# Kernel tuning notes

Hardware: AMD Instinct MI355X
Metric: run time of the kernel (lower is better)

The kernel has to match this reference:

```python
import jax, jax.numpy as jnp
import numpy as np

B, N, C, F, OUT = 4, 512, 1024, 1024, 1024
LOC = 128  # min(128, out_channels)
EPS_BN = 1e-5


def _batchnorm(x, g, b):
    # BatchNorm1d in training mode: biased batch stats over rows
    m = jnp.mean(x, axis=0)
    v = jnp.var(x, axis=0)
    return (x - m) / jnp.sqrt(v + EPS_BN) * g + b


def _relative_pe(loc):
    # loc: [N,4] (x,y,w,h) -> [N,N,LOC]; faithfully replicates the torch
    # cat([N,4N]) -> view(-1,4) interleaving of the original code.
    cx = loc[:, 0] + 0.5 * loc[:, 2]
    cy = loc[:, 1] + 0.5 * loc[:, 3]
    w, h = loc[:, 2], loc[:, 3]
    eps = jnp.float32(1e-3)
    dx = jnp.maximum(jnp.abs(cx[:, None] - cx[None, :]) / w[None, :], eps)
    dy = jnp.maximum(jnp.abs(cy[:, None] - cy[None, :]) / h[None, :], eps)
    dw = w[:, None] / w[None, :]
    dh = h[:, None] / h[None, :]
    delta = jnp.log(jnp.concatenate([dx, dy, dw, dh], axis=-1))  # [N,4N]
    delta = delta.reshape(-1, 4)                                  # [N*N,4]
    d = LOC // 8
    pe = jnp.exp(2.0 * jnp.arange(d, dtype=jnp.float32) / d * np.log(1000.0))
    ang = delta[:, :, None] / pe                                  # [N*N,4,d]
    emb = jnp.concatenate([jnp.sin(ang), jnp.cos(ang)], axis=-1)  # [N*N,4,2d]
    return emb.reshape(N, N, LOC)


def reference(box_features, boxes, bn1_g, bn1_b, Wq, bq, Wk, bk, Wv, bv, Wr, br, bn2_g, bn2_b):
    feat = _batchnorm(box_features, bn1_g, bn1_b).reshape(B, N, C)

    def per_image(f, loc):
        rel = jnp.squeeze(_relative_pe(loc) @ Wr + br, axis=-1)   # [N,N]
        q = f @ Wq + bq
        k = f @ Wk + bk
        v = f @ Wv + bv
        att = q @ k.T / jnp.sqrt(jnp.float32(F)) + jax.nn.log_softmax(rel, axis=-1)
        return jax.nn.softmax(att, axis=-1) @ v                   # [N,OUT]

    out = jax.vmap(per_image)(feat, boxes).reshape(B * N, OUT)
    return _batchnorm(out, bn2_g, bn2_b)


def setup_inputs() -> dict:
    key = jax.random.key(0)
    ks = jax.random.split(key, 10)
    box_features = jax.random.normal(ks[0], (B * N, C), dtype=jnp.float32)
    u = jax.random.uniform(ks[1], (B, N, 4), dtype=jnp.float32)
    xy = u[..., :2] * 800.0
    wh = 16.0 + u[..., 2:] * 240.0
    boxes = jnp.concatenate([xy, wh], axis=-1)
    s = 0.02
    return {
        "box_features": box_features,
        "boxes": boxes,
        "bn1_g": jnp.ones((C,), jnp.float32),
        "bn1_b": jnp.zeros((C,), jnp.float32),
        "Wq": jax.random.normal(ks[2], (C, F), jnp.float32) * s,
        "bq": jnp.zeros((F,), jnp.float32),
        "Wk": jax.random.normal(ks[3], (C, F), jnp.float32) * s,
        "bk": jnp.zeros((F,), jnp.float32),
        "Wv": jax.random.normal(ks[4], (C, OUT), jnp.float32) * s,
        "bv": jnp.zeros((OUT,), jnp.float32),
        "Wr": jax.random.normal(ks[5], (LOC, 1), jnp.float32) * s,
        "br": jnp.zeros((1,), jnp.float32),
        "bn2_g": jnp.ones((OUT,), jnp.float32),
        "bn2_b": jnp.zeros((OUT,), jnp.float32),
    }
```

## Files before the change

kernel.cpp:

```cpp
#include <hip/hip_runtime.h>
#include <math.h>

typedef __bf16 bf16;
typedef __attribute__((ext_vector_type(8))) __bf16 bf16x8;
typedef __attribute__((ext_vector_type(4))) __bf16 bf16x4;
typedef __attribute__((ext_vector_type(4))) float f32x4;

#define NCH1 128
#define RPC1 16

#define XD0   (-6.93f)
#define XSPAN (11.03f)
#define XINVH (1023.f / 11.03f)

__global__ __launch_bounds__(256)
void prep(const float* __restrict__ Wq, const float* __restrict__ Wk, const float* __restrict__ Wv,
          bf16* __restrict__ T0, bf16* __restrict__ T1, bf16* __restrict__ T2,
          const float* __restrict__ bq, const float* __restrict__ bk, float* __restrict__ biasqk,
          const float* __restrict__ X, float* __restrict__ psum, float* __restrict__ psq,
          const float* __restrict__ boxes, const float* __restrict__ Wr, const float* __restrict__ br,
          float* __restrict__ ent, float* __restrict__ tabs)
{
    __shared__ float tile[64][65];
    const int bid = blockIdx.x;
    const int tid = threadIdx.x;

    if (bid < 768) {
        const int mat = bid >> 8, g2 = bid & 255;
        const float* W = (mat == 0) ? Wq : (mat == 1) ? Wk : Wv;
        bf16* T        = (mat == 0) ? T0 : (mat == 1) ? T1 : T2;
        const int bx = (g2 & 15) * 64, by = (g2 >> 4) * 64;
        const int tx = tid & 63, ty = tid >> 6;
#pragma unroll
        for (int i = 0; i < 16; ++i)
            tile[ty + i * 4][tx] = W[(long)(by + ty + i * 4) * 1024 + bx + tx];
        __syncthreads();
#pragma unroll
        for (int i = 0; i < 16; ++i)
            T[(long)(bx + ty + i * 4) * 1024 + by + tx] = (bf16)tile[tx][ty + i * 4];
    } else if (bid < 896) {
        const int c4 = tid;
        const long r0 = (long)(bid - 768) * RPC1;
        const float4* Xv = (const float4*)X;
        float4 s = {0.f,0.f,0.f,0.f}, q = {0.f,0.f,0.f,0.f};
#pragma unroll
        for (int r = 0; r < RPC1; ++r) {
            float4 x = Xv[(r0 + r) * 256 + c4];
            s.x += x.x; s.y += x.y; s.z += x.z; s.w += x.w;
            q.x += x.x*x.x; q.y += x.y*x.y; q.z += x.z*x.z; q.w += x.w*x.w;
        }
        ((float4*)psum)[(bid - 768) * 256 + c4] = s;
        ((float4*)psq) [(bid - 768) * 256 + c4] = q;
    } else if (bid == 896) {
        for (int e = tid; e < 2048; e += 256) {
            float4 b4 = ((const float4*)boxes)[e];
            float w = b4.z, h = b4.w;
            ent[0*2048+e] = b4.x + 0.5f * w;
            ent[1*2048+e] = b4.y + 0.5f * h;
            ent[2*2048+e] = __logf(w);
            ent[3*2048+e] = __logf(h);
            ent[4*2048+e] = 1e-3f * w;
            ent[5*2048+e] = 1e-3f * h;
        }
        for (int i = tid; i < 2048; i += 256)
            biasqk[i] = (i < 1024) ? bq[i] : bk[i - 1024];
    } else {
        const int c = bid - 897;
        float* tb = tabs + c * 1024;
        const float brq = 0.25f * br[0];
        const float hstep = XSPAN / 1023.f;
        for (int e = tid; e < 1024; e += 256) {
            float d = XD0 + hstep * (float)e;
            float a = brq;
#pragma unroll
            for (int k = 0; k < 16; ++k) {
                float tk = exp2f(-1.24572303558f * (float)k);
                float s_, c_;
                __sincosf(d * tk, &s_, &c_);
                a += s_ * Wr[c * 32 + k] + c_ * Wr[c * 32 + 16 + k];
            }
            tb[e] = a;
        }
    }
}

template <int NCH_, int BF16OUT>
__global__ __launch_bounds__(256)
void bn_final_apply(const float* __restrict__ X, const float* __restrict__ psum,
                    const float* __restrict__ psq, const float* __restrict__ g,
                    const float* __restrict__ b, void* __restrict__ Yp)
{
    __shared__ float ls[4][64], lq[4][64], ssc[64], ssh[64];
    const int t  = threadIdx.x;
    const int cs = blockIdx.x;
    const int rc = blockIdx.y;
    const int col_l = t & 63, part = t >> 6;
    const int col = cs * 64 + col_l;
    constexpr int CPT = NCH_ / 4;
    float s = 0.f, q = 0.f;
#pragma unroll
    for (int i = 0; i < CPT; ++i) {
        int ch = part * CPT + i;
        s += psum[ch * 1024 + col];
        q += psq [ch * 1024 + col];
    }
    ls[part][col_l] = s; lq[part][col_l] = q;
    __syncthreads();
    if (t < 64) {
        float S = ls[0][t]+ls[1][t]+ls[2][t]+ls[3][t];
        float Q = lq[0][t]+lq[1][t]+lq[2][t]+lq[3][t];
        float m = S / 2048.f;
        float v = Q / 2048.f - m*m;
        float inv = 1.0f / sqrtf(v + 1e-5f);
        float sc = g[cs*64+t] * inv;
        ssc[t] = sc; ssh[t] = b[cs*64+t] - m*sc;
    }
    __syncthreads();
    const int f = t & 15, rsub = t >> 4;
    float4 sc4 = ((const float4*)ssc)[f];
    float4 sh4 = ((const float4*)ssh)[f];
#pragma unroll
    for (int it = 0; it < 8; ++it) {
        int row = rc*128 + it*16 + rsub;
        float4 x = ((const float4*)(X + (long)row*1024 + cs*64))[f];
        float4 rv;
        rv.x = x.x*sc4.x + sh4.x;
        rv.y = x.y*sc4.y + sh4.y;
        rv.z = x.z*sc4.z + sh4.z;
        rv.w = x.w*sc4.w + sh4.w;
        if constexpr (BF16OUT) {
            bf16x4 y;
            y[0]=(bf16)rv.x; y[1]=(bf16)rv.y; y[2]=(bf16)rv.z; y[3]=(bf16)rv.w;
            ((bf16x4*)((bf16*)Yp + (long)row*1024 + cs*64))[f] = y;
        } else {
            ((float4*)((float*)Yp + (long)row*1024 + cs*64))[f] = rv;
        }
    }
}

__device__ __forceinline__ float look(const float* tab, float d)
{
    float t = (d - XD0) * XINVH;
    t = fminf(fmaxf(t, 0.f), 1022.999f);
    float fi = floorf(t);
    int i = (int)fi;
    float a = tab[i], b = tab[i + 1];
    return a + (b - a) * (t - fi);
}

__device__ __forceinline__ void stage_tile_128x32(const bf16* __restrict__ src_base, int ld,
                                                  int row0, int k0, bf16* lds_base, int w, int l)
{
#pragma unroll
    for (int t = 0; t < 2; ++t) {
        int rchunk = w * 32 + t * 16;
        const bf16* src = src_base + (long)(row0 + rchunk + (l >> 2)) * ld + k0 + (l & 3) * 8;
        __builtin_amdgcn_global_load_lds((__attribute__((address_space(1))) void*)src,
                                         (__attribute__((address_space(3))) void*)(lds_base + rchunk * 32),
                                         16, 0, 0);
    }
}

__device__ __forceinline__ void stage64(const bf16* __restrict__ src_base, int ld,
                                        int row0, int k0, bf16* lds_base, int w, int l)
{
    const bf16* src = src_base + (long)(row0 + w * 16 + (l >> 2)) * ld + k0 + (l & 3) * 8;
    __builtin_amdgcn_global_load_lds((__attribute__((address_space(1))) void*)src,
                                     (__attribute__((address_space(3))) void*)(lds_base + w * 16 * 32),
                                     16, 0, 0);
}

template <int MODE>
__device__ __forceinline__ void gemm_12864(
    const bf16* __restrict__ Ab, int lda, const bf16* __restrict__ Bb, int ldb,
    bf16* __restrict__ Cp, int ldc, int K, int bm, int bn,
    const float* __restrict__ bias, char* smem)
{
    bf16* As0 = (bf16*)smem;
    bf16* Bs0 = (bf16*)(smem + 16384);
    const int tid = threadIdx.x;
    const int w = tid >> 6, l = tid & 63;
    const int wr = w >> 1, wc = w & 1;

    f32x4 acc[4][2];
#pragma unroll
    for (int i = 0; i < 4; ++i)
#pragma unroll
        for (int j = 0; j < 2; ++j) acc[i][j] = (f32x4){0.f,0.f,0.f,0.f};

    const int nkt = K >> 5;
    stage_tile_128x32(Ab, lda, bm, 0, As0, w, l);
    stage64(Bb, ldb, bn, 0, Bs0, w, l);
    __syncthreads();

    const int fr = l & 15;
    const int ko = (l >> 4) * 8;

    for (int kt = 0; kt < nkt; ++kt) {
        const int cur = kt & 1;
        bf16* Asc = As0 + cur * 4096;
        bf16* Bsc = Bs0 + cur * 2048;
        if (kt + 1 < nkt) {
            stage_tile_128x32(Ab, lda, bm, (kt + 1) << 5, As0 + (cur ^ 1) * 4096, w, l);
            stage64(Bb, ldb, bn, (kt + 1) << 5, Bs0 + (cur ^ 1) * 2048, w, l);
        }
        bf16x8 af[4], bfv[2];
#pragma unroll
        for (int mi = 0; mi < 4; ++mi)
            af[mi] = *(const bf16x8*)(&Asc[(wr * 64 + mi * 16 + fr) * 32 + ko]);
#pragma unroll
        for (int ni = 0; ni < 2; ++ni)
            bfv[ni] = *(const bf16x8*)(&Bsc[(wc * 32 + ni * 16 + fr) * 32 + ko]);
#pragma unroll
        for (int mi = 0; mi < 4; ++mi)
#pragma unroll
            for (int ni = 0; ni < 2; ++ni)
                acc[mi][ni] = __builtin_amdgcn_mfma_f32_16x16x32_bf16(af[mi], bfv[ni], acc[mi][ni], 0, 0, 0);
        __syncthreads();
    }

    const int crow0 = bm + wr * 64 + (l >> 4) * 4;
    const int ccol0 = bn + wc * 32 + fr;
#pragma unroll
    for (int mi = 0; mi < 4; ++mi)
#pragma unroll
        for (int ni = 0; ni < 2; ++ni)
#pragma unroll
            for (int r = 0; r < 4; ++r) {
                const int row = crow0 + mi * 16 + r;
                const int col = ccol0 + ni * 16;
                const float v = acc[mi][ni][r];
                if constexpr (MODE == 0) {
                    Cp[(long)row * ldc + col] = (bf16)(v + bias[col]);
                } else {
                    Cp[(long)row * ldc + col] = (bf16)(v + bias[row]);
                }
            }
}

__global__ __launch_bounds__(256, 4)
void megaGEMM(const bf16* __restrict__ featbf, const bf16* __restrict__ WqkT,
              const bf16* __restrict__ WvT, bf16* __restrict__ qkbf, bf16* __restrict__ vTbf,
              const float* __restrict__ biasqk, const float* __restrict__ bv)
{
    __shared__ char smem[24576];
    const unsigned bid = blockIdx.x;
    const unsigned g = bid / 3u, r = bid % 3u;
    if (r < 2) {
        const unsigned t = g * 2 + r;
        gemm_12864<0>(featbf, 1024, WqkT, 1024, qkbf, 2048, 1024,
                      (t & 15) * 128, (t >> 4) * 64, biasqk, smem);
    } else {
        const int img = g >> 6, rem = g & 63;
        gemm_12864<1>(WvT, 1024, featbf + (long)img * 524288,  1024,
                      vTbf + (long)img * 524288, 512, 1024,
                      (rem >> 3) * 128, (rem & 7) * 64, bv, smem);
    }
}

__global__ __launch_bounds__(256, 4)
void attn64(const bf16* __restrict__ qk, float* __restrict__ S0, float* __restrict__ S1,
            const float* __restrict__ ent, const float* __restrict__ tabs)
{
    __shared__ char smem[20480];
    const int img = blockIdx.z >> 1, kh = blockIdx.z & 1;
    const int bm = blockIdx.x * 64, bn = blockIdx.y * 64;
    const bf16* A = qk + (long)img * 1048576 + kh * 512;
    const bf16* B = qk + 1024 + (long)img * 1048576 + kh * 512;
    bf16* As0 = (bf16*)smem;
    bf16* Bs0 = (bf16*)(smem + 8192);

    const int tid = threadIdx.x;
    const int w = tid >> 6, l = tid & 63;
    const int wr = w >> 1, wc = w & 1;
    const int fr = l & 15;
    const int ko = (l >> 4) * 8;

    f32x4 acc[2][2];
#pragma unroll
    for (int i = 0; i < 2; ++i)
#pragma unroll
        for (int j = 0; j < 2; ++j) acc[i][j] = (f32x4){0.f,0.f,0.f,0.f};

    stage64(A, 2048, bm, 0, As0, w, l);
    stage64(B, 2048, bn, 0, Bs0, w, l);
    __syncthreads();

    for (int kt = 0; kt < 16; ++kt) {
        const int cur = kt & 1;
        bf16* Asc = As0 + cur * 2048;
        bf16* Bsc = Bs0 + cur * 2048;
        if (kt + 1 < 16) {
            stage64(A, 2048, bm, (kt + 1) << 5, As0 + (cur ^ 1) * 2048, w, l);
            stage64(B, 2048, bn, (kt + 1) << 5, Bs0 + (cur ^ 1) * 2048, w, l);
        }
        bf16x8 af[2], bfv[2];
#pragma unroll
        for (int mi = 0; mi < 2; ++mi)
            af[mi] = *(const bf16x8*)(&Asc[(wr * 32 + mi * 16 + fr) * 32 + ko]);
#pragma unroll
        for (int ni = 0; ni < 2; ++ni)
            bfv[ni] = *(const bf16x8*)(&Bsc[(wc * 32 + ni * 16 + fr) * 32 + ko]);
#pragma unroll
        for (int mi = 0; mi < 2; ++mi)
#pragma unroll
            for (int ni = 0; ni < 2; ++ni)
                acc[mi][ni] = __builtin_amdgcn_mfma_f32_16x16x32_bf16(af[mi], bfv[ni], acc[mi][ni], 0, 0, 0);
        __syncthreads();
    }

    const float scale = 0.03125f;
    float* Sout = (kh == 0 ? S0 : S1) + (long)img * 262144;

    if (kh == 1) {
#pragma unroll
        for (int mi = 0; mi < 2; ++mi)
#pragma unroll
            for (int ni = 0; ni < 2; ++ni)
#pragma unroll
                for (int r = 0; r < 4; ++r) {
                    const int rowl = wr * 32 + mi * 16 + (l >> 4) * 4 + r;
                    const int coll = wc * 32 + ni * 16 + fr;
                    Sout[(long)(bm + rowl) * 512 + bn + coll] = acc[mi][ni][r] * scale;
                }
        return;
    }

    float* stab = (float*)smem;
    float* RA   = stab + 4096;
    float* SA   = RA + 64;
    float* SE   = SA + 260;
    float* SL   = SE + 260;
    const int b   = bn >> 7;
    const int jj0 = (bn & 64) * 4;
    for (int i = tid; i < 4096; i += 256) stab[i] = tabs[i];
    {
        const int eb = img * 512;
        if (tid < 64) RA[tid] = ent[b * 2048 + eb + bm + tid];
        for (int u = tid; u < 260 && jj0 + u < 512; u += 256) {
            SA[u] = ent[b * 2048 + eb + jj0 + u];
            if (b < 2) {
                SE[u] = ent[(4 + b) * 2048 + eb + jj0 + u];
                SL[u] = ent[(2 + b) * 2048 + eb + jj0 + u];
            }
        }
    }
    __syncthreads();
#pragma unroll
    for (int ni = 0; ni < 2; ++ni) {
        const int coll = wc * 32 + ni * 16 + fr;
        const int u0   = 4 * coll;
        const float sA0 = SA[u0], sA1 = SA[u0+1], sA2 = SA[u0+2], sA3 = SA[u0+3];
        float sE0=0.f,sE1=0.f,sE2=0.f,sE3=0.f, sL0=0.f,sL1=0.f,sL2=0.f,sL3=0.f;
        if (b < 2) {
            sE0 = SE[u0]; sE1 = SE[u0+1]; sE2 = SE[u0+2]; sE3 = SE[u0+3];
            sL0 = SL[u0]; sL1 = SL[u0+1]; sL2 = SL[u0+2]; sL3 = SL[u0+3];
        }
#pragma unroll
        for (int mi = 0; mi < 2; ++mi)
#pragma unroll
            for (int r = 0; r < 4; ++r) {
                const int rowl = wr * 32 + mi * 16 + (l >> 4) * 4 + r;
                const float ai = RA[rowl];
                float d0, d1, d2, d3;
                if (b < 2) {
                    d0 = __logf(fmaxf(fabsf(ai - sA0), sE0)) - sL0;
                    d1 = __logf(fmaxf(fabsf(ai - sA1), sE1)) - sL1;
                    d2 = __logf(fmaxf(fabsf(ai - sA2), sE2)) - sL2;
                    d3 = __logf(fmaxf(fabsf(ai - sA3), sE3)) - sL3;
                } else {
                    d0 = ai - sA0; d1 = ai - sA1; d2 = ai - sA2; d3 = ai - sA3;
                }
                float relv = look(stab,        d0) + look(stab + 1024, d1)
                           + look(stab + 2048, d2) + look(stab + 3072, d3);
                Sout[(long)(bm + rowl) * 512 + bn + coll] = acc[mi][ni][r] * scale + relv;
            }
    }
}

__global__ __launch_bounds__(256)
void softmax2(const float* __restrict__ S0, const float* __restrict__ S1, bf16* __restrict__ P)
{
    const long row = blockIdx.x;
    const int t = threadIdx.x;
    float x0 = S0[row * 512 + t]       + S1[row * 512 + t];
    float x1 = S0[row * 512 + t + 256] + S1[row * 512 + t + 256];
    float mx = fmaxf(x0, x1);
#pragma unroll
    for (int off = 32; off; off >>= 1) mx = fmaxf(mx, __shfl_xor(mx, off));
    __shared__ float redm[4], reds[4];
    if ((t & 63) == 0) redm[t >> 6] = mx;
    __syncthreads();
    mx = fmaxf(fmaxf(redm[0], redm[1]), fmaxf(redm[2], redm[3]));
    float e0 = __expf(x0 - mx), e1 = __expf(x1 - mx);
    float sm = e0 + e1;
#pragma unroll
    for (int off = 32; off; off >>= 1) sm += __shfl_xor(sm, off);
    if ((t & 63) == 0) reds[t >> 6] = sm;
    __syncthreads();
    sm = (reds[0] + reds[1]) + (reds[2] + reds[3]);
    float inv = 1.0f / sm;
    P[row * 512 + t]       = (bf16)(e0 * inv);
    P[row * 512 + t + 256] = (bf16)(e1 * inv);
}

__global__ __launch_bounds__(256, 4)
void pv64(const bf16* __restrict__ P, const bf16* __restrict__ vT, float* __restrict__ out,
          float* __restrict__ psum, float* __restrict__ psq)
{
    __shared__ char smem[16384];
    const int img = blockIdx.z;
    const int bm = blockIdx.x * 64, bn = blockIdx.y * 64;
    const bf16* A = P  + (long)img * 262144;
    const bf16* B = vT + (long)img * 524288;
    float* C = out + (long)img * 524288;
    bf16* As0 = (bf16*)smem;
    bf16* Bs0 = (bf16*)(smem + 8192);

    const int tid = threadIdx.x;
    const int w = tid >> 6, l = tid & 63;
    const int wr = w >> 1, wc = w & 1;
    const int fr = l & 15;
    const int ko = (l >> 4) * 8;

    f32x4 acc[2][2];
#pragma unroll
    for (int i = 0; i < 2; ++i)
#pragma unroll
        for (int j = 0; j < 2; ++j) acc[i][j] = (f32x4){0.f,0.f,0.f,0.f};

    stage64(A, 512, bm, 0, As0, w, l);
    stage64(B, 512, bn, 0, Bs0, w, l);
    __syncthreads();

    for (int kt = 0; kt < 16; ++kt) {
        const int cur = kt & 1;
        bf16* Asc = As0 + cur * 2048;
        bf16* Bsc = Bs0 + cur * 2048;
        if (kt + 1 < 16) {
            stage64(A, 512, bm, (kt + 1) << 5, As0 + (cur ^ 1) * 2048, w, l);
            stage64(B, 512, bn, (kt + 1) << 5, Bs0 + (cur ^ 1) * 2048, w, l);
        }
        bf16x8 af[2], bfv[2];
#pragma unroll
        for (int mi = 0; mi < 2; ++mi)
            af[mi] = *(const bf16x8*)(&Asc[(wr * 32 + mi * 16 + fr) * 32 + ko]);
#pragma unroll
        for (int ni = 0; ni < 2; ++ni)
            bfv[ni] = *(const bf16x8*)(&Bsc[(wc * 32 + ni * 16 + fr) * 32 + ko]);
#pragma unroll
        for (int mi = 0; mi < 2; ++mi)
#pragma unroll
            for (int ni = 0; ni < 2; ++ni)
                acc[mi][ni] = __builtin_amdgcn_mfma_f32_16x16x32_bf16(af[mi], bfv[ni], acc[mi][ni], 0, 0, 0);
        __syncthreads();
    }

#pragma unroll
    for (int mi = 0; mi < 2; ++mi)
#pragma unroll
        for (int ni = 0; ni < 2; ++ni)
#pragma unroll
            for (int r = 0; r < 4; ++r) {
                const int rowl = wr * 32 + mi * 16 + (l >> 4) * 4 + r;
                const int coll = wc * 32 + ni * 16 + fr;
                C[(long)(bm + rowl) * 1024 + bn + coll] = acc[mi][ni][r];
            }

    float s_[2], q_[2];
#pragma unroll
    for (int ni = 0; ni < 2; ++ni) {
        float s = 0.f, q = 0.f;
#pragma unroll
        for (int mi = 0; mi < 2; ++mi)
#pragma unroll
            for (int r = 0; r < 4; ++r) { float v = acc[mi][ni][r]; s += v; q += v * v; }
        s_[ni] = s; q_[ni] = q;
    }
#pragma unroll
    for (int ni = 0; ni < 2; ++ni) {
        s_[ni] += __shfl_xor(s_[ni], 16); s_[ni] += __shfl_xor(s_[ni], 32);
        q_[ni] += __shfl_xor(q_[ni], 16); q_[ni] += __shfl_xor(q_[ni], 32);
    }
    float* lred = (float*)smem;
    __syncthreads();
    if (l < 16) {
#pragma unroll
        for (int ni = 0; ni < 2; ++ni) {
            const int c = wc * 32 + ni * 16 + l;
            lred[(wr * 2 + 0) * 64 + c] = s_[ni];
            lred[(wr * 2 + 1) * 64 + c] = q_[ni];
        }
    }
    __syncthreads();
    if (tid < 64) {
        const int chunk = img * 8 + blockIdx.x;
        psum[chunk * 1024 + bn + tid] = lred[0 * 64 + tid] + lred[2 * 64 + tid];
        psq [chunk * 1024 + bn + tid] = lred[1 * 64 + tid] + lred[3 * 64 + tid];
    }
}

extern "C" void kernel_launch(void* const* d_in, const int* in_sizes, int n_in,
                              void* d_out, int out_size, void* d_ws, size_t ws_size,
                              hipStream_t stream)
{
    const float* box_features = (const float*)d_in[0];
    const float* boxes  = (const float*)d_in[1];
    const float* bn1_g  = (const float*)d_in[2];
    const float* bn1_b  = (const float*)d_in[3];
    const float* Wq     = (const float*)d_in[4];
    const float* bq     = (const float*)d_in[5];
    const float* Wk     = (const float*)d_in[6];
    const float* bk     = (const float*)d_in[7];
    const float* Wv     = (const float*)d_in[8];
    const float* bv     = (const float*)d_in[9];
    const float* Wr     = (const float*)d_in[10];
    const float* br     = (const float*)d_in[11];
    const float* bn2_g  = (const float*)d_in[12];
    const float* bn2_b  = (const float*)d_in[13];
    float* out = (float*)d_out;

    char* ws = (char*)d_ws;
    const long MB = 1024 * 1024;
    float* psum   = (float*)(ws + 0);
    float* psq    = (float*)(ws + 512 * 1024);
    float* biasqk = (float*)(ws + 1 * MB);
    float* ent    = (float*)(ws + 1 * MB + 65536);
    float* tabs   = (float*)(ws + 1 * MB + 131072);
    bf16*  featbf = (bf16*)(ws + 2 * MB);
    bf16*  WqkT   = (bf16*)(ws + 6 * MB);
    float* Sbuf1  = (float*)(ws + 6 * MB);
    bf16*  WvT    = (bf16*)(ws + 10 * MB);
    bf16*  qkbf   = (bf16*)(ws + 12 * MB);
    bf16*  vTbf   = (bf16*)(ws + 20 * MB);
    float* Sbuf0  = (float*)(ws + 24 * MB);
    bf16*  Pbuf   = (bf16*)(ws + 28 * MB);

    prep<<<dim3(901, 1, 1), dim3(256, 1, 1), 0, stream>>>(
        Wq, Wk, Wv, WqkT, WqkT + 1024 * 1024, WvT, bq, bk, biasqk,
        box_features, psum, psq, boxes, Wr, br, ent, tabs);

    bn_final_apply<NCH1, 1><<<dim3(16, 16, 1), dim3(256, 1, 1), 0, stream>>>(
        box_features, psum, psq, bn1_g, bn1_b, featbf);

    megaGEMM<<<dim3(768, 1, 1), dim3(256, 1, 1), 0, stream>>>(
        featbf, WqkT, WvT, qkbf, vTbf, biasqk, bv);

    attn64<<<dim3(8, 8, 8), dim3(256, 1, 1), 0, stream>>>(qkbf, Sbuf0, Sbuf1, ent, tabs);

    softmax2<<<dim3(2048, 1, 1), dim3(256, 1, 1), 0, stream>>>(Sbuf0, Sbuf1, Pbuf);

    pv64<<<dim3(8, 16, 4), dim3(256, 1, 1), 0, stream>>>(Pbuf, vTbf, out, psum, psq);

    bn_final_apply<32, 0><<<dim3(16, 16, 1), dim3(256, 1, 1), 0, stream>>>(
        out, psum, psq, bn2_g, bn2_b, out);
}
```

Baseline: 90.22 us.

## Fold Wq·Wkᵀ into one matrix so attention scores use features directly

Precomputes G = Wk·Wqᵀ (a 1024x1024 bf16 product) inside the prep kernel, plus a per-row vector wvec = Wk·bq. The projection GEMM then computes t = feat·G + wvec instead of separate Q and K, and the attention score GEMM multiplies t by feat directly. The bk term is dropped because it only adds a per-row constant that softmax cancels. This halves the projection GEMM output and removes the Wq/Wk transposes, at the cost of a 1024^3 GEMM in prep that runs serially before the rest, and some extra bf16 rounding.

```diff
diff --git a/kernel.cpp b/kernel.cpp
--- a/kernel.cpp
+++ b/kernel.cpp
@@ -15,32 +15,30 @@
 
 __global__ __launch_bounds__(256)
 void prep(const float* __restrict__ Wq, const float* __restrict__ Wk, const float* __restrict__ Wv,
-          bf16* __restrict__ T0, bf16* __restrict__ T1, bf16* __restrict__ T2,
-          const float* __restrict__ bq, const float* __restrict__ bk, float* __restrict__ biasqk,
+          bf16* __restrict__ WvT, const float* __restrict__ bq,
           const float* __restrict__ X, float* __restrict__ psum, float* __restrict__ psq,
           const float* __restrict__ boxes, const float* __restrict__ Wr, const float* __restrict__ br,
-          float* __restrict__ ent, float* __restrict__ tabs)
-{
-    __shared__ float tile[64][65];
+          float* __restrict__ ent, float* __restrict__ tabs,
+          bf16* __restrict__ GT, float* __restrict__ wvec)
+{
+    __shared__ char psm[24576];
     const int bid = blockIdx.x;
     const int tid = threadIdx.x;
 
-    if (bid < 768) {
-        const int mat = bid >> 8, g2 = bid & 255;
-        const float* W = (mat == 0) ? Wq : (mat == 1) ? Wk : Wv;
-        bf16* T        = (mat == 0) ? T0 : (mat == 1) ? T1 : T2;
-        const int bx = (g2 & 15) * 64, by = (g2 >> 4) * 64;
+    if (bid < 256) {
+        float (*tile)[65] = (float(*)[65])psm;
+        const int bx = (bid & 15) * 64, by = (bid >> 4) * 64;
         const int tx = tid & 63, ty = tid >> 6;
 #pragma unroll
         for (int i = 0; i < 16; ++i)
-            tile[ty + i * 4][tx] = W[(long)(by + ty + i * 4) * 1024 + bx + tx];
+            tile[ty + i * 4][tx] = Wv[(long)(by + ty + i * 4) * 1024 + bx + tx];
         __syncthreads();
 #pragma unroll
         for (int i = 0; i < 16; ++i)
-            T[(long)(bx + ty + i * 4) * 1024 + by + tx] = (bf16)tile[tx][ty + i * 4];
-    } else if (bid < 896) {
+            WvT[(long)(bx + ty + i * 4) * 1024 + by + tx] = (bf16)tile[tx][ty + i * 4];
+    } else if (bid < 384) {
         const int c4 = tid;
-        const long r0 = (long)(bid - 768) * RPC1;
+        const long r0 = (long)(bid - 256) * RPC1;
         const float4* Xv = (const float4*)X;
         float4 s = {0.f,0.f,0.f,0.f}, q = {0.f,0.f,0.f,0.f};
 #pragma unroll
@@ -49,9 +47,9 @@
             s.x += x.x; s.y += x.y; s.z += x.z; s.w += x.w;
             q.x += x.x*x.x; q.y += x.y*x.y; q.z += x.z*x.z; q.w += x.w*x.w;
         }
-        ((float4*)psum)[(bid - 768) * 256 + c4] = s;
-        ((float4*)psq) [(bid - 768) * 256 + c4] = q;
-    } else if (bid == 896) {
+        ((float4*)psum)[(bid - 256) * 256 + c4] = s;
+        ((float4*)psq) [(bid - 256) * 256 + c4] = q;
+    } else if (bid == 384) {
         for (int e = tid; e < 2048; e += 256) {
             float4 b4 = ((const float4*)boxes)[e];
             float w = b4.z, h = b4.w;
@@ -62,10 +60,8 @@
             ent[4*2048+e] = 1e-3f * w;
             ent[5*2048+e] = 1e-3f * h;
         }
-        for (int i = tid; i < 2048; i += 256)
-            biasqk[i] = (i < 1024) ? bq[i] : bk[i - 1024];
-    } else {
-        const int c = bid - 897;
+    } else if (bid < 389) {
+        const int c = bid - 385;
         float* tb = tabs + c * 1024;
         const float brq = 0.25f * br[0];
         const float hstep = XSPAN / 1023.f;
@@ -80,6 +76,91 @@
                 a += s_ * Wr[c * 32 + k] + c_ * Wr[c * 32 + 16 + k];
             }
             tb[e] = a;
+        }
+    } else {
+        const int b2 = bid - 389;
+        const int m0 = (b2 >> 4) * 128;
+        const int n0 = (b2 & 15) * 64;
+        bf16* As0 = (bf16*)psm;
+        bf16* Bs0 = (bf16*)(psm + 16384);
+        const int w4 = tid >> 6, l = tid & 63;
+        const int wr = w4 >> 1, wc = w4 & 1;
+        const int fr = l & 15, ko = (l >> 4) * 8;
+        const int ra = tid >> 1, ka = (tid & 1) * 16;
+        const int rb = tid >> 2, kb = (tid & 3) * 8;
+
+        f32x4 acc[4][2];
+#pragma unroll
+        for (int i = 0; i < 4; ++i)
+#pragma unroll
+            for (int j = 0; j < 2; ++j) acc[i][j] = (f32x4){0.f,0.f,0.f,0.f};
+        float wacc = 0.f;
+
+        auto stgA = [&](int k0, bf16* dst) {
+            const float* s = Wk + (long)(m0 + ra) * 1024 + k0 + ka;
+            float4 x0 = *(const float4*)s,     x1 = *(const float4*)(s + 4);
+            float4 x2 = *(const float4*)(s + 8), x3 = *(const float4*)(s + 12);
+            bf16x8 y0, y1;
+            y0[0]=(bf16)x0.x; y0[1]=(bf16)x0.y; y0[2]=(bf16)x0.z; y0[3]=(bf16)x0.w;
+            y0[4]=(bf16)x1.x; y0[5]=(bf16)x1.y; y0[6]=(bf16)x1.z; y0[7]=(bf16)x1.w;
+            y1[0]=(bf16)x2.x; y1[1]=(bf16)x2.y; y1[2]=(bf16)x2.z; y1[3]=(bf16)x2.w;
+            y1[4]=(bf16)x3.x; y1[5]=(bf16)x3.y; y1[6]=(bf16)x3.z; y1[7]=(bf16)x3.w;
+            *(bf16x8*)(dst + ra * 32 + ka)     = y0;
+            *(bf16x8*)(dst + ra * 32 + ka + 8) = y1;
+        };
+        auto stgB = [&](int k0, bf16* dst) {
+            const float* s = Wq + (long)(n0 + rb) * 1024 + k0 + kb;
+            float4 x0 = *(const float4*)s, x1 = *(const float4*)(s + 4);
+            bf16x8 y;
+            y[0]=(bf16)x0.x; y[1]=(bf16)x0.y; y[2]=(bf16)x0.z; y[3]=(bf16)x0.w;
+            y[4]=(bf16)x1.x; y[5]=(bf16)x1.y; y[6]=(bf16)x1.z; y[7]=(bf16)x1.w;
+            *(bf16x8*)(dst + rb * 32 + kb) = y;
+        };
+
+        stgA(0, As0); stgB(0, Bs0);
+        __syncthreads();
+        for (int kt = 0; kt < 32; ++kt) {
+            const int cur = kt & 1;
+            bf16* Asc = As0 + cur * 4096;
+            bf16* Bsc = Bs0 + cur * 2048;
+            if (kt + 1 < 32) {
+                stgA((kt + 1) * 32, As0 + (cur ^ 1) * 4096);
+                stgB((kt + 1) * 32, Bs0 + (cur ^ 1) * 2048);
+            }
+            bf16x8 af[4], bfv[2];
+#pragma unroll
+            for (int mi = 0; mi < 4; ++mi)
+                af[mi] = *(const bf16x8*)(&Asc[(wr * 64 + mi * 16 + fr) * 32 + ko]);
+#pragma unroll
+            for (int ni = 0; ni < 2; ++ni)
+                bfv[ni] = *(const bf16x8*)(&Bsc[(wc * 32 + ni * 16 + fr) * 32 + ko]);
+#pragma unroll
+            for (int mi = 0; mi < 4; ++mi)
+#pragma unroll
+                for (int ni = 0; ni < 2; ++ni)
+                    acc[mi][ni] = __builtin_amdgcn_mfma_f32_16x16x32_bf16(af[mi], bfv[ni], acc[mi][ni], 0, 0, 0);
+            if ((b2 & 15) == 0) {
+                const bf16* arow = Asc + ra * 32 + ka;
+                const float* bqp = bq + kt * 32 + ka;
+#pragma unroll
+                for (int u = 0; u < 16; ++u) wacc += (float)arow[u] * bqp[u];
+            }
+            __syncthreads();
+        }
+
+        const int crow0 = m0 + wr * 64 + (l >> 4) * 4;
+        const int ccol0 = n0 + wc * 32 + fr;
+#pragma unroll
+        for (int mi = 0; mi < 4; ++mi)
+#pragma unroll
+            for (int ni = 0; ni < 2; ++ni)
+#pragma unroll
+                for (int r = 0; r < 4; ++r)
+                    GT[(long)(crow0 + mi * 16 + r) * 1024 + ccol0 + ni * 16] = (bf16)acc[mi][ni][r];
+
+        if ((b2 & 15) == 0) {
+            wacc += __shfl_xor(wacc, 1);
+            if ((tid & 1) == 0) wvec[m0 + ra] = wacc;
         }
     }
 }
@@ -239,34 +320,35 @@
 }
 
 __global__ __launch_bounds__(256, 4)
-void megaGEMM(const bf16* __restrict__ featbf, const bf16* __restrict__ WqkT,
-              const bf16* __restrict__ WvT, bf16* __restrict__ qkbf, bf16* __restrict__ vTbf,
-              const float* __restrict__ biasqk, const float* __restrict__ bv)
+void megaGEMM(const bf16* __restrict__ featbf, const bf16* __restrict__ GT,
+              const bf16* __restrict__ WvT, bf16* __restrict__ tbf, bf16* __restrict__ vTbf,
+              const float* __restrict__ wvec, const float* __restrict__ bv)
 {
     __shared__ char smem[24576];
     const unsigned bid = blockIdx.x;
-    const unsigned g = bid / 3u, r = bid % 3u;
-    if (r < 2) {
-        const unsigned t = g * 2 + r;
-        gemm_12864<0>(featbf, 1024, WqkT, 1024, qkbf, 2048, 1024,
-                      (t & 15) * 128, (t >> 4) * 64, biasqk, smem);
+    const int half = bid & 1;
+    const unsigned g = bid >> 1;
+    if (half == 0) {
+        gemm_12864<0>(featbf, 1024, GT, 1024, tbf, 1024, 1024,
+                      (g & 15) * 128, (g >> 4) * 64, wvec, smem);
     } else {
         const int img = g >> 6, rem = g & 63;
-        gemm_12864<1>(WvT, 1024, featbf + (long)img * 524288,  1024,
+        gemm_12864<1>(WvT, 1024, featbf + (long)img * 524288, 1024,
                       vTbf + (long)img * 524288, 512, 1024,
                       (rem >> 3) * 128, (rem & 7) * 64, bv, smem);
     }
 }
 
 __global__ __launch_bounds__(256, 4)
-void attn64(const bf16* __restrict__ qk, float* __restrict__ S0, float* __restrict__ S1,
+void attn64(const bf16* __restrict__ tbf, const bf16* __restrict__ featbf,
+            float* __restrict__ S0, float* __restrict__ S1,
             const float* __restrict__ ent, const float* __restrict__ tabs)
 {
     __shared__ char smem[20480];
     const int img = blockIdx.z >> 1, kh = blockIdx.z & 1;
     const int bm = blockIdx.x * 64, bn = blockIdx.y * 64;
-    const bf16* A = qk + (long)img * 1048576 + kh * 512;
-    const bf16* B = qk + 1024 + (long)img * 1048576 + kh * 512;
+    const bf16* A = tbf    + (long)img * 524288 + kh * 512;
+    const bf16* B = featbf + (long)img * 524288 + kh * 512;
     bf16* As0 = (bf16*)smem;
     bf16* Bs0 = (bf16*)(smem + 8192);
 
@@ -282,8 +364,8 @@
 #pragma unroll
         for (int j = 0; j < 2; ++j) acc[i][j] = (f32x4){0.f,0.f,0.f,0.f};
 
-    stage64(A, 2048, bm, 0, As0, w, l);
-    stage64(B, 2048, bn, 0, Bs0, w, l);
+    stage64(A, 1024, bm, 0, As0, w, l);
+    stage64(B, 1024, bn, 0, Bs0, w, l);
     __syncthreads();
 
     for (int kt = 0; kt < 16; ++kt) {
@@ -291,8 +373,8 @@
         bf16* Asc = As0 + cur * 2048;
         bf16* Bsc = Bs0 + cur * 2048;
         if (kt + 1 < 16) {
-            stage64(A, 2048, bm, (kt + 1) << 5, As0 + (cur ^ 1) * 2048, w, l);
-            stage64(B, 2048, bn, (kt + 1) << 5, Bs0 + (cur ^ 1) * 2048, w, l);
+            stage64(A, 1024, bm, (kt + 1) << 5, As0 + (cur ^ 1) * 2048, w, l);
+            stage64(B, 1024, bn, (kt + 1) << 5, Bs0 + (cur ^ 1) * 2048, w, l);
         }
         bf16x8 af[2], bfv[2];
 #pragma unroll
@@ -519,34 +601,34 @@
     const float* bn2_g  = (const float*)d_in[12];
     const float* bn2_b  = (const float*)d_in[13];
     float* out = (float*)d_out;
+    (void)bk;
 
     char* ws = (char*)d_ws;
     const long MB = 1024 * 1024;
     float* psum   = (float*)(ws + 0);
     float* psq    = (float*)(ws + 512 * 1024);
-    float* biasqk = (float*)(ws + 1 * MB);
-    float* ent    = (float*)(ws + 1 * MB + 65536);
-    float* tabs   = (float*)(ws + 1 * MB + 131072);
+    float* ent    = (float*)(ws + 1 * MB);
+    float* tabs   = (float*)(ws + 1 * MB + 65536);
+    float* wvec   = (float*)(ws + 1 * MB + 131072);
     bf16*  featbf = (bf16*)(ws + 2 * MB);
-    bf16*  WqkT   = (bf16*)(ws + 6 * MB);
-    float* Sbuf1  = (float*)(ws + 6 * MB);
-    bf16*  WvT    = (bf16*)(ws + 10 * MB);
-    bf16*  qkbf   = (bf16*)(ws + 12 * MB);
-    bf16*  vTbf   = (bf16*)(ws + 20 * MB);
-    float* Sbuf0  = (float*)(ws + 24 * MB);
-    bf16*  Pbuf   = (bf16*)(ws + 28 * MB);
-
-    prep<<<dim3(901, 1, 1), dim3(256, 1, 1), 0, stream>>>(
-        Wq, Wk, Wv, WqkT, WqkT + 1024 * 1024, WvT, bq, bk, biasqk,
-        box_features, psum, psq, boxes, Wr, br, ent, tabs);
+    bf16*  GT     = (bf16*)(ws + 6 * MB);
+    bf16*  WvT    = (bf16*)(ws + 8 * MB);
+    bf16*  tbf    = (bf16*)(ws + 10 * MB);
+    bf16*  vTbf   = (bf16*)(ws + 14 * MB);
+    float* Sbuf0  = (float*)(ws + 18 * MB);
+    float* Sbuf1  = (float*)(ws + 22 * MB);
+    bf16*  Pbuf   = (bf16*)(ws + 26 * MB);
+
+    prep<<<dim3(517, 1, 1), dim3(256, 1, 1), 0, stream>>>(
+        Wq, Wk, Wv, WvT, bq, box_features, psum, psq, boxes, Wr, br, ent, tabs, GT, wvec);
 
     bn_final_apply<NCH1, 1><<<dim3(16, 16, 1), dim3(256, 1, 1), 0, stream>>>(
         box_features, psum, psq, bn1_g, bn1_b, featbf);
 
-    megaGEMM<<<dim3(768, 1, 1), dim3(256, 1, 1), 0, stream>>>(
-        featbf, WqkT, WvT, qkbf, vTbf, biasqk, bv);
-
-    attn64<<<dim3(8, 8, 8), dim3(256, 1, 1), 0, stream>>>(qkbf, Sbuf0, Sbuf1, ent, tabs);
+    megaGEMM<<<dim3(512, 1, 1), dim3(256, 1, 1), 0, stream>>>(
+        featbf, GT, WvT, tbf, vTbf, wvec, bv);
+
+    attn64<<<dim3(8, 8, 8), dim3(256, 1, 1), 0, stream>>>(tbf, featbf, Sbuf0, Sbuf1, ent, tabs);
 
     softmax2<<<dim3(2048, 1, 1), dim3(256, 1, 1), 0, stream>>>(Sbuf0, Sbuf1, Pbuf);
 
```

New measurement: 110.5 us. +22.4%, slower.
